# Optimization experiments

Measured on AMD Instinct MI355X. Metric: run time of the kernel, lower is better.

## Reference

```python
import jax, jax.numpy as jnp
import numpy as np

D, DFF, H, K = 512, 2048, 8, 31
DK = D // H
EPS = 1e-5


def _ln(x, g, b):
    m = jnp.mean(x, axis=-1, keepdims=True)
    v = jnp.mean((x - m) ** 2, axis=-1, keepdims=True)
    return (x - m) * jax.lax.rsqrt(v + EPS) * g + b


def _ffn(x, w1, b1, w2, b2):
    return jax.nn.silu(x @ w1 + b1) @ w2 + b2


def _rel_shift(x):
    # x: (B, H, T, P) with P = 2T-1
    b, h, q, p = x.shape
    x = jnp.pad(x, ((0, 0), (0, 0), (0, 0), (1, 0)))
    x = x.reshape(b, h, p + 1, q)[:, :, 1:, :]
    return x.reshape(b, h, q, p)


def setup_inputs() -> dict:
    key = jax.random.key(0)
    ks = jax.random.split(key, 32)
    r = lambda i, shape: 0.02 * jax.random.normal(ks[i], shape, dtype=jnp.float32)
    B, T = 4, 1024
    inp = {
        'x': jax.random.normal(ks[0], (B, T, D), dtype=jnp.float32),
        'pos_emb': jax.random.normal(ks[1], (1, 2 * T - 1, D), dtype=jnp.float32),
        # LayerNorms (5)
        'ln1_g': jnp.ones((D,)), 'ln1_b': jnp.zeros((D,)),
        'ln2_g': jnp.ones((D,)), 'ln2_b': jnp.zeros((D,)),
        'ln3_g': jnp.ones((D,)), 'ln3_b': jnp.zeros((D,)),
        'ln4_g': jnp.ones((D,)), 'ln4_b': jnp.zeros((D,)),
        'ln5_g': jnp.ones((D,)), 'ln5_b': jnp.zeros((D,)),
        # FFN1
        'ff1_w1': r(2, (D, DFF)), 'ff1_b1': jnp.zeros((DFF,)),
        'ff1_w2': r(3, (DFF, D)), 'ff1_b2': jnp.zeros((D,)),
        # Attention
        'wq': r(4, (D, D)), 'bq': jnp.zeros((D,)),
        'wk': r(5, (D, D)), 'bk': jnp.zeros((D,)),
        'wv': r(6, (D, D)), 'bv': jnp.zeros((D,)),
        'wp': r(7, (D, D)),
        'wo': r(8, (D, D)), 'bo': jnp.zeros((D,)),
        'pos_u': r(9, (H, DK)), 'pos_v': r(10, (H, DK)),
        # Conv module
        'pw1_w': r(11, (2 * D, D)), 'pw1_b': jnp.zeros((2 * D,)),
        'dw_w': r(12, (D, 1, K)), 'dw_b': jnp.zeros((D,)),
        'bn_g': jnp.ones((D,)), 'bn_b': jnp.zeros((D,)),
        'pw2_w': r(13, (D, D)), 'pw2_b': jnp.zeros((D,)),
        # FFN2
        'ff2_w1': r(14, (D, DFF)), 'ff2_b1': jnp.zeros((DFF,)),
        'ff2_w2': r(15, (DFF, D)), 'ff2_b2': jnp.zeros((D,)),
    }
    return inp


def _attn(x, pos_emb, wq, bq, wk, bk, wv, bv, wp, wo, bo, pos_u, pos_v):
    B, T, _ = x.shape
    q = (x @ wq + bq).reshape(B, T, H, DK).transpose(0, 2, 1, 3)
    k = (x @ wk + bk).reshape(B, T, H, DK).transpose(0, 2, 1, 3)
    v = (x @ wv + bv).reshape(B, T, H, DK).transpose(0, 2, 1, 3)
    P = pos_emb.shape[1]
    p = (pos_emb[0] @ wp).reshape(P, H, DK)  # (P, H, DK)
    ac = jnp.einsum('bhqd,bhkd->bhqk', q + pos_u[:, None, :], k)
    bd = jnp.einsum('bhqd,phd->bhqp', q + pos_v[:, None, :], p)
    bd = _rel_shift(bd)[:, :, :, :T]
    scores = (ac + bd) * (DK ** -0.5)
    attn = jax.nn.softmax(scores, axis=-1)
    out = jnp.einsum('bhqk,bhkd->bhqd', attn, v)
    out = out.transpose(0, 2, 1, 3).reshape(B, T, D)
    return out @ wo + bo


def _conv(x, pw1_w, pw1_b, dw_w, dw_b, bn_g, bn_b, pw2_w, pw2_b):
    y = x.transpose(0, 2, 1)  # (B, D, T)
    y = jnp.einsum('od,bdt->bot', pw1_w, y) + pw1_b[:, None]
    a, g = jnp.split(y, 2, axis=1)
    y = a * jax.nn.sigmoid(g)  # GLU
    pad = (K - 1) // 2
    y = jax.lax.conv_general_dilated(
        y, dw_w, (1,), [(pad, pad)],
        dimension_numbers=('NCW', 'OIW', 'NCW'), feature_group_count=D)
    y = y + dw_b[:, None]
    m = jnp.mean(y, axis=(0, 2), keepdims=True)
    var = jnp.mean((y - m) ** 2, axis=(0, 2), keepdims=True)
    y = (y - m) * jax.lax.rsqrt(var + EPS) * bn_g[:, None] + bn_b[:, None]
    y = jax.nn.silu(y)
    y = jnp.einsum('od,bdt->bot', pw2_w, y) + pw2_b[:, None]
    return y.transpose(0, 2, 1)


def reference(x, pos_emb,
              ln1_g, ln1_b, ff1_w1, ff1_b1, ff1_w2, ff1_b2,
              ln2_g, ln2_b, wq, bq, wk, bk, wv, bv, wp, wo, bo, pos_u, pos_v,
              ln3_g, ln3_b, pw1_w, pw1_b, dw_w, dw_b, bn_g, bn_b, pw2_w, pw2_b,
              ln4_g, ln4_b, ff2_w1, ff2_b1, ff2_w2, ff2_b2,
              ln5_g, ln5_b):
    h = x + 0.5 * _ffn(_ln(x, ln1_g, ln1_b), ff1_w1, ff1_b1, ff1_w2, ff1_b2)
    h = h + _attn(_ln(h, ln2_g, ln2_b), pos_emb, wq, bq, wk, bk, wv, bv, wp, wo, bo, pos_u, pos_v)
    h = h + _conv(_ln(h, ln3_g, ln3_b), pw1_w, pw1_b, dw_w, dw_b, bn_g, bn_b, pw2_w, pw2_b)
    h = h + 0.5 * _ffn(_ln(h, ln4_g, ln4_b), ff2_w1, ff2_b1, ff2_w2, ff2_b2)
    return _ln(h, ln5_g, ln5_b)
```

## Files before the change

### kernel.cpp

```cpp
#include <hip/hip_runtime.h>
#include <math.h>

#define TT   1024
#define BBZ  4
#define DD   512
#define DFF_ 2048
#define HH   8
#define DKK  64
#define NTOK 4096
#define EPSF 1e-5f
#define MB   1048576

typedef unsigned short u16;
typedef __attribute__((ext_vector_type(8))) short s8v;
typedef __attribute__((ext_vector_type(4))) float f32x4;
typedef __attribute__((ext_vector_type(4))) unsigned short us4;

__device__ __forceinline__ float b2f(u16 v){
    union { unsigned int u; float f; } x; x.u = ((unsigned int)v) << 16; return x.f;
}
__device__ __forceinline__ u16 f2b(float f){
    union { float f; unsigned int u; } x; x.f = f;
    unsigned int r = x.u + 0x7fffu + ((x.u >> 16) & 1u);
    return (u16)(r >> 16);
}
__device__ __forceinline__ float sigmoidf_(float x){ return 1.0f/(1.0f+__expf(-x)); }

__device__ __forceinline__ void gld16(const u16* g, u16* l){
    __builtin_amdgcn_global_load_lds(
        (const __attribute__((address_space(1))) unsigned int*)g,
        (__attribute__((address_space(3))) unsigned int*)l, 16, 0, 0);
}

template<int OMODE>
__global__ __launch_bounds__(256) void bgemm128(
    const u16* __restrict__ A, int lda,
    const u16* __restrict__ B, int ldb,
    void* __restrict__ Cv, int ldc, int K,
    const float* __restrict__ bias, int act, float alpha,
    const float* __restrict__ resid,
    const float* __restrict__ posu, const float* __restrict__ posv)
{
    int n0 = blockIdx.x * 128;
    int m0 = blockIdx.y * 128;

    __shared__ u16 As[128*64];
    __shared__ u16 Bs[128*64];

    int t = threadIdx.x;
    int w = t >> 6, l = t & 63;
    int lrow = l >> 3, lslot = l & 7;
    int kswz = (lslot ^ lrow) * 8;
    int wm = w >> 1, wn = w & 1;
    int lr = l & 15, lk = l >> 4;

    f32x4 acc[4][4] = {};

    for (int k0 = 0; k0 < K; k0 += 64){
        #pragma unroll
        for (int it = 0; it < 4; ++it){
            int rb = it*32 + w*8;
            gld16(A + (size_t)(m0 + rb + lrow)*lda + k0 + kswz, &As[rb*64]);
            gld16(B + (size_t)(n0 + rb + lrow)*ldb + k0 + kswz, &Bs[rb*64]);
        }
        __syncthreads();

        s8v af[2][4], bf[2][4];
        #pragma unroll
        for (int kh = 0; kh < 2; ++kh){
            int sl = (kh*4 + lk) ^ (lr & 7);
            #pragma unroll
            for (int mi = 0; mi < 4; ++mi)
                af[kh][mi] = *(const s8v*)&As[(wm*64 + mi*16 + lr)*64 + sl*8];
            #pragma unroll
            for (int ni = 0; ni < 4; ++ni)
                bf[kh][ni] = *(const s8v*)&Bs[(wn*64 + ni*16 + lr)*64 + sl*8];
        }
        #pragma unroll
        for (int kh = 0; kh < 2; ++kh)
            #pragma unroll
            for (int mi = 0; mi < 4; ++mi)
                #pragma unroll
                for (int ni = 0; ni < 4; ++ni)
                    acc[mi][ni] = __builtin_amdgcn_mfma_f32_16x16x32_bf16(
                        af[kh][mi], bf[kh][ni], acc[mi][ni], 0, 0, 0);
        __syncthreads();
    }

    #pragma unroll
    for (int mi = 0; mi < 4; ++mi){
        #pragma unroll
        for (int ni = 0; ni < 4; ++ni){
            int gn = n0 + wn*64 + ni*16 + lr;
            float bval = bias ? bias[gn] : 0.0f;
            #pragma unroll
            for (int r = 0; r < 4; ++r){
                int gm = m0 + wm*64 + mi*16 + lk*4 + r;
                float vv = acc[mi][ni][r] + bval;
                if (act) vv = vv * sigmoidf_(vv);
                if (OMODE == 0){
                    vv *= alpha;
                    if (resid) vv += resid[(size_t)gm*ldc + gn];
                    ((float*)Cv)[(size_t)gm*ldc + gn] = vv;
                } else if (OMODE == 1){
                    ((u16*)Cv)[(size_t)gm*ldc + gn] = f2b(vv);
                } else {
                    u16* base = (u16*)Cv;
                    if (gn < 512){
                        size_t idx = (size_t)gm*512 + gn;
                        base[idx]              = f2b((vv + posu[gn])*0.125f);
                        base[idx + (2u<<20)]   = f2b((vv + posv[gn])*0.125f);
                    } else if (gn < 1024){
                        base[(4u<<20) + (size_t)gm*512 + (gn-512)] = f2b(vv);
                    } else {
                        int gnp = gn - 1024;
                        int bb = gm >> 10, tt2 = gm & 1023;
                        size_t idx = (((size_t)(bb*8 + (gnp>>6)))*64 + (gnp&63))*1024 + tt2;
                        base[(6u<<20) + idx] = f2b(vv);
                    }
                }
            }
        }
    }
}

template<int OMODE>
__global__ __launch_bounds__(256) void bgemm64(
    const u16* __restrict__ A, int lda,
    const u16* __restrict__ B, int ldb,
    void* __restrict__ Cv, int ldc, int K,
    const float* __restrict__ bias, float alpha,
    const float* __restrict__ resid)
{
    int n0 = blockIdx.x * 64;
    int m0 = blockIdx.y * 64;

    __shared__ u16 As[64*64];
    __shared__ u16 Bs[64*64];

    int t = threadIdx.x;
    int w = t >> 6, l = t & 63;
    int lrow = l >> 3, lslot = l & 7;
    int kswz = (lslot ^ lrow) * 8;
    int wm = w >> 1, wn = w & 1;
    int lr = l & 15, lk = l >> 4;

    f32x4 acc[2][2] = {};

    for (int k0 = 0; k0 < K; k0 += 64){
        #pragma unroll
        for (int it = 0; it < 2; ++it){
            int rb = it*32 + w*8;
            gld16(A + (size_t)(m0 + rb + lrow)*lda + k0 + kswz, &As[rb*64]);
            gld16(B + (size_t)(n0 + rb + lrow)*ldb + k0 + kswz, &Bs[rb*64]);
        }
        __syncthreads();

        s8v af[2][2], bf[2][2];
        #pragma unroll
        for (int kh = 0; kh < 2; ++kh){
            int sl = (kh*4 + lk) ^ (lr & 7);
            #pragma unroll
            for (int mi = 0; mi < 2; ++mi)
                af[kh][mi] = *(const s8v*)&As[(wm*32 + mi*16 + lr)*64 + sl*8];
            #pragma unroll
            for (int ni = 0; ni < 2; ++ni)
                bf[kh][ni] = *(const s8v*)&Bs[(wn*32 + ni*16 + lr)*64 + sl*8];
        }
        #pragma unroll
        for (int kh = 0; kh < 2; ++kh)
            #pragma unroll
            for (int mi = 0; mi < 2; ++mi)
                #pragma unroll
                for (int ni = 0; ni < 2; ++ni)
                    acc[mi][ni] = __builtin_amdgcn_mfma_f32_16x16x32_bf16(
                        af[kh][mi], bf[kh][ni], acc[mi][ni], 0, 0, 0);
        __syncthreads();
    }

    #pragma unroll
    for (int mi = 0; mi < 2; ++mi){
        #pragma unroll
        for (int ni = 0; ni < 2; ++ni){
            int gn = n0 + wn*32 + ni*16 + lr;
            float bval = bias ? bias[gn] : 0.0f;
            #pragma unroll
            for (int r = 0; r < 4; ++r){
                int gm = m0 + wm*32 + mi*16 + lk*4 + r;
                float vv = acc[mi][ni][r] + bval;
                if (OMODE == 0){
                    vv *= alpha;
                    if (resid) vv += resid[(size_t)gm*ldc + gn];
                    ((float*)Cv)[(size_t)gm*ldc + gn] = vv;
                } else {
                    ((u16*)Cv)[(size_t)gm*ldc + gn] = f2b(vv);
                }
            }
        }
    }
}

__global__ __launch_bounds__(256) void attn_fused(
    const u16* __restrict__ qub, const u16* __restrict__ qvb,
    const u16* __restrict__ kb,  const u16* __restrict__ vt,
    const u16* __restrict__ pp,  u16* __restrict__ out)
{
    int z = blockIdx.y;
    int b = z >> 3, hh = z & 7;
    int i0 = blockIdx.x * 64;

    __shared__ u16 Kb2[2][64*64];
    __shared__ u16 Pring[3][64*64];
    __shared__ u16 Vb[64*64];
    __shared__ u16 PT[64*64];
    __shared__ float Band[64*64];

    int t = threadIdx.x;
    int w = t >> 6, l = t & 63;
    int lrow = l >> 3, lslot = l & 7;
    int kswz = (lslot ^ lrow) * 8;
    int lr = l & 15, lk = l >> 4;

    #pragma unroll
    for (int it = 0; it < 2; ++it){
        int rb = it*32 + w*8;
        gld16(qub + (size_t)(b*TT + i0 + rb + lrow)*DD + hh*64 + kswz, &Vb[rb*64]);
        gld16(qvb + (size_t)(b*TT + i0 + rb + lrow)*DD + hh*64 + kswz, &PT[rb*64]);
    }
    __syncthreads();
    s8v af_u[2], af_v[2];
    #pragma unroll
    for (int kh = 0; kh < 2; ++kh){
        int sl = (kh*4 + lk) ^ (lr & 7);
        af_u[kh] = *(const s8v*)&Vb[(w*16 + lr)*64 + sl*8];
        af_v[kh] = *(const s8v*)&PT[(w*16 + lr)*64 + sl*8];
    }
    #pragma unroll
    for (int it = 0; it < 2; ++it){
        int rb = it*32 + w*8;
        gld16(kb + (size_t)(b*TT +        rb + lrow)*DD + hh*64 + kswz, &Kb2[0][rb*64]);
        gld16(pp + (size_t)(960  - i0 +   rb + lrow)*DD + hh*64 + kswz, &Pring[0][rb*64]);
        gld16(pp + (size_t)(1024 - i0 +   rb + lrow)*DD + hh*64 + kswz, &Pring[1][rb*64]);
    }

    f32x4 o_[4] = {};
    float M_[4], L_[4];
    #pragma unroll
    for (int r = 0; r < 4; ++r){ M_[r] = -3e38f; L_[r] = 0.0f; }

    int nbase = 3 - w;
    int s0 = 0, s1 = 1, s2 = 2;

    for (int jt = 0; jt < 16; ++jt){
        int cur = jt & 1;
        __syncthreads();

        #pragma unroll
        for (int it = 0; it < 2; ++it){
            int rb = it*32 + w*8;
            gld16(vt + ((size_t)z*64 + rb + lrow)*TT + jt*64 + kswz, &Vb[rb*64]);
            if (jt < 15){
                gld16(kb + (size_t)(b*TT + (jt+1)*64 + rb + lrow)*DD + hh*64 + kswz,
                      &Kb2[cur^1][rb*64]);
                gld16(pp + (size_t)(960 + (jt+2)*64 - i0 + rb + lrow)*DD + hh*64 + kswz,
                      &Pring[s2][rb*64]);
            }
        }

        f32x4 sac[4] = {};
        f32x4 g[5] = {};
        #pragma unroll
        for (int kh = 0; kh < 2; ++kh){
            int sl = (kh*4 + lk) ^ (lr & 7);
            #pragma unroll
            for (int n = 0; n < 4; ++n){
                s8v bK = *(const s8v*)&Kb2[cur][(n*16 + lr)*64 + sl*8];
                sac[n] = __builtin_amdgcn_mfma_f32_16x16x32_bf16(af_u[kh], bK, sac[n], 0,0,0);
            }
            #pragma unroll
            for (int n = 0; n < 5; ++n){
                int nn = nbase + n;
                const u16* pc = (nn & 4) ? &Pring[s1][0] : &Pring[s0][0];
                s8v bP = *(const s8v*)&pc[(((nn&3)*16) + lr)*64 + sl*8];
                g[n] = __builtin_amdgcn_mfma_f32_16x16x32_bf16(af_v[kh], bP, g[n], 0,0,0);
            }
        }
        #pragma unroll
        for (int n = 0; n < 5; ++n){
            int nn = nbase + n;
            #pragma unroll
            for (int r = 0; r < 4; ++r){
                int ii = w*16 + lk*4 + r;
                int jj = nn*16 + lr - 63 + ii;
                if (jj >= 0 && jj < 64)
                    Band[ii*64 + ((jj + 4*ii) & 63)] = g[n][r];
            }
        }

        float p_[4][4], sc_[4];
        #pragma unroll
        for (int r = 0; r < 4; ++r){
            int ii = w*16 + lk*4 + r;
            float sv[4]; float mx = -3e38f;
            #pragma unroll
            for (int n = 0; n < 4; ++n){
                int jj = n*16 + lr;
                float vvv = sac[n][r] + Band[ii*64 + ((jj + 4*ii) & 63)];
                sv[n] = vvv; mx = fmaxf(mx, vvv);
            }
            #pragma unroll
            for (int msk = 1; msk < 16; msk <<= 1) mx = fmaxf(mx, __shfl_xor(mx, msk));
            float nm = fmaxf(M_[r], mx);
            float scale = __expf(M_[r] - nm);
            float rs = 0.0f;
            #pragma unroll
            for (int n = 0; n < 4; ++n){ p_[n][r] = __expf(sv[n] - nm); rs += p_[n][r]; }
            #pragma unroll
            for (int msk = 1; msk < 16; msk <<= 1) rs += __shfl_xor(rs, msk);
            L_[r] = L_[r]*scale + rs;
            M_[r] = nm;
            sc_[r] = scale;
        }
        #pragma unroll
        for (int n = 0; n < 4; ++n)
            #pragma unroll
            for (int r = 0; r < 4; ++r)
                o_[n][r] *= sc_[r];

        #pragma unroll
        for (int n = 0; n < 4; ++n)
            #pragma unroll
            for (int r = 0; r < 4; ++r){
                int ii  = w*16 + lk*4 + r;
                int col = n*16 + lr;
                int sl  = (col>>3) ^ (ii&7);
                PT[ii*64 + sl*8 + (col&7)] = f2b(p_[n][r]);
            }

        __syncthreads();

        #pragma unroll
        for (int kh = 0; kh < 2; ++kh){
            int sl = (kh*4 + lk) ^ (lr & 7);
            s8v ap = *(const s8v*)&PT[(w*16 + lr)*64 + sl*8];
            #pragma unroll
            for (int n = 0; n < 4; ++n){
                s8v bV = *(const s8v*)&Vb[(n*16 + lr)*64 + sl*8];
                o_[n] = __builtin_amdgcn_mfma_f32_16x16x32_bf16(ap, bV, o_[n], 0,0,0);
            }
        }
        int tmp = s0; s0 = s1; s1 = s2; s2 = tmp;
    }

    #pragma unroll
    for (int n = 0; n < 4; ++n)
        #pragma unroll
        for (int r = 0; r < 4; ++r){
            int i  = i0 + w*16 + lk*4 + r;
            int dk = n*16 + lr;
            out[(size_t)(b*TT + i)*DD + hh*64 + dk] = f2b(o_[n][r] / L_[r]);
        }
}

template<int OB>
__global__ __launch_bounds__(256) void ln_kernel(const float* __restrict__ in,
    const float* __restrict__ g, const float* __restrict__ b, void* __restrict__ outv)
{
    int w = threadIdx.x >> 6, l = threadIdx.x & 63;
    int row = blockIdx.x*4 + w;
    const float4* xr = (const float4*)(in + (size_t)row*DD);
    float4 v0 = xr[l], v1 = xr[64 + l];
    float s = v0.x+v0.y+v0.z+v0.w + v1.x+v1.y+v1.z+v1.w;
    float q = v0.x*v0.x+v0.y*v0.y+v0.z*v0.z+v0.w*v0.w
            + v1.x*v1.x+v1.y*v1.y+v1.z*v1.z+v1.w*v1.w;
    #pragma unroll
    for (int msk = 1; msk < 64; msk <<= 1){
        s += __shfl_xor(s, msk);
        q += __shfl_xor(q, msk);
    }
    float mean = s*(1.0f/DD);
    float var  = q*(1.0f/DD) - mean*mean;
    float inv  = rsqrtf(var+EPSF);
    float4 g0 = ((const float4*)g)[l], g1 = ((const float4*)g)[64+l];
    float4 b0 = ((const float4*)b)[l], b1 = ((const float4*)b)[64+l];
    float y0x=(v0.x-mean)*inv*g0.x+b0.x, y0y=(v0.y-mean)*inv*g0.y+b0.y;
    float y0z=(v0.z-mean)*inv*g0.z+b0.z, y0w=(v0.w-mean)*inv*g0.w+b0.w;
    float y1x=(v1.x-mean)*inv*g1.x+b1.x, y1y=(v1.y-mean)*inv*g1.y+b1.y;
    float y1z=(v1.z-mean)*inv*g1.z+b1.z, y1w=(v1.w-mean)*inv*g1.w+b1.w;
    if (OB){
        us4 o0 = { f2b(y0x), f2b(y0y), f2b(y0z), f2b(y0w) };
        us4 o1 = { f2b(y1x), f2b(y1y), f2b(y1z), f2b(y1w) };
        us4* op = (us4*)((u16*)outv + (size_t)row*DD);
        op[l] = o0; op[64+l] = o1;
    } else {
        float4 o0 = { y0x, y0y, y0z, y0w };
        float4 o1 = { y1x, y1y, y1z, y1w };
        float4* op = (float4*)((float*)outv + (size_t)row*DD);
        op[l] = o0; op[64+l] = o1;
    }
}

struct Prep9 {
    const float* s[9];
    u16* d[9];
    int R[9], C[9];
    int t0[10];
};

__global__ __launch_bounds__(256) void prep_transpose(Prep9 P)
{
    __shared__ float tile[32][33];
    int bid = blockIdx.x;
    int j = 0;
    #pragma unroll
    for (int e=1; e<9; e++) if (bid >= P.t0[e]) j = e;
    int lb = bid - P.t0[j];
    int nx = P.C[j] >> 5;
    int c0 = (lb % nx) << 5;
    int r0 = (lb / nx) << 5;
    const float* in = P.s[j];
    u16* out = P.d[j];
    int R = P.R[j], C = P.C[j];
    int tx = threadIdx.x & 31, ty = threadIdx.x >> 5;
    #pragma unroll
    for (int i=0;i<4;i++){
        int rr = ty + i*8;
        tile[rr][tx] = in[(size_t)(r0+rr)*C + c0+tx];
    }
    __syncthreads();
    #pragma unroll
    for (int i=0;i<4;i++){
        int cc = ty + i*8;
        out[(size_t)(c0+cc)*R + r0+tx] = f2b(tile[tx][cc]);
    }
}

__global__ __launch_bounds__(256) void prep_convert(
    const float* __restrict__ pw1_w, const float* __restrict__ pw2_w,
    const float* __restrict__ pos_emb, const float* __restrict__ dw_w,
    const float* __restrict__ bq, const float* __restrict__ bk,
    const float* __restrict__ bv,
    u16* __restrict__ pw1b, u16* __restrict__ pw2b,
    u16* __restrict__ posb, float* __restrict__ wt, float* __restrict__ bqkv)
{
    int i = blockIdx.x*256 + threadIdx.x;
    if (i < 524288) { pw1b[i] = f2b(pw1_w[i]); return; }
    i -= 524288;
    if (i < 262144) { pw2b[i] = f2b(pw2_w[i]); return; }
    i -= 262144;
    if (i < 1048576) { posb[i] = (i < 2047*512) ? f2b(pos_emb[i]) : (u16)0; return; }
    i -= 1048576;
    if (i < 15872) { int kk = i >> 9, d = i & 511; wt[i] = dw_w[d*31+kk]; return; }
    i -= 15872;
    if (i < 1536) bqkv[i] = (i < 512) ? bq[i] : (i < 1024 ? bk[i-512] : bv[i-1024]);
}

__global__ __launch_bounds__(256) void dwconv_kernel(const float* __restrict__ t2,
    const float* __restrict__ wt, const float* __restrict__ bias, float* __restrict__ z)
{
    int d  = blockIdx.x*256 + threadIdx.x;
    int c  = blockIdx.y;
    int b  = c >> 7;
    int t0 = (c & 127) << 3;
    const float* pa = t2 + (size_t)b*TT*1024 + d;
    float wv[31];
    #pragma unroll
    for (int kk=0;kk<31;kk++) wv[kk] = wt[kk*512 + d];
    float xv[38];
    #pragma unroll
    for (int e=0;e<38;e++){
        int tp = t0 - 15 + e;
        if (tp >= 0 && tp < TT){
            float a  = pa[(size_t)tp*1024];
            float gg = pa[(size_t)tp*1024 + 512];
            xv[e] = a * sigmoidf_(gg);
        } else xv[e] = 0.0f;
    }
    float bsv = bias[d];
    #pragma unroll
    for (int j=0;j<8;j++){
        float sum = bsv;
        #pragma unroll
        for (int kk=0;kk<31;kk++) sum = fmaf(xv[j+kk], wv[kk], sum);
        z[(size_t)(b*TT+t0+j)*DD + d] = sum;
    }
}

__global__ __launch_bounds__(256) void bn_reduce_kernel(const float* __restrict__ z, float* __restrict__ stats)
{
    int c = blockIdx.x, t = threadIdx.x;
    float s=0.f, q=0.f;
    for (int r=t; r<NTOK; r+=256){
        float vv = z[(size_t)r*DD + c];
        s += vv; q += vv*vv;
    }
    __shared__ float rs[256], rq[256];
    rs[t]=s; rq[t]=q; __syncthreads();
    for (int st=128; st>0; st>>=1){
        if (t<st){ rs[t]+=rs[t+st]; rq[t]+=rq[t+st]; }
        __syncthreads();
    }
    if (t==0){ stats[c]=rs[0]; stats[DD+c]=rq[0]; }
}

__global__ __launch_bounds__(256) void bn_apply_kernel(const float* __restrict__ z,
    const float* __restrict__ stats, const float* __restrict__ g, const float* __restrict__ b,
    u16* __restrict__ out)
{
    int idx = blockIdx.x*256 + threadIdx.x;
    int c = idx & (DD-1);
    float m   = stats[c]*(1.0f/NTOK);
    float var = stats[DD+c]*(1.0f/NTOK) - m*m;
    float vv  = (z[idx]-m)*rsqrtf(var+EPSF)*g[c] + b[c];
    out[idx]  = f2b(vv*sigmoidf_(vv));
}

extern "C" void kernel_launch(void* const* d_in, const int* in_sizes, int n_in,
                              void* d_out, int out_size, void* d_ws, size_t ws_size,
                              hipStream_t stream)
{
    const float* x       = (const float*)d_in[0];
    const float* pos_emb = (const float*)d_in[1];
    const float* ln1_g=(const float*)d_in[2],  *ln1_b=(const float*)d_in[3];
    const float* ln2_g=(const float*)d_in[4],  *ln2_b=(const float*)d_in[5];
    const float* ln3_g=(const float*)d_in[6],  *ln3_b=(const float*)d_in[7];
    const float* ln4_g=(const float*)d_in[8],  *ln4_b=(const float*)d_in[9];
    const float* ln5_g=(const float*)d_in[10], *ln5_b=(const float*)d_in[11];
    const float* ff1_w1=(const float*)d_in[12], *ff1_b1=(const float*)d_in[13];
    const float* ff1_w2=(const float*)d_in[14], *ff1_b2=(const float*)d_in[15];
    const float* wq=(const float*)d_in[16], *bq=(const float*)d_in[17];
    const float* wk=(const float*)d_in[18], *bk=(const float*)d_in[19];
    const float* wv=(const float*)d_in[20], *bv=(const float*)d_in[21];
    const float* wp=(const float*)d_in[22];
    const float* wo=(const float*)d_in[23], *bo=(const float*)d_in[24];
    const float* pos_u=(const float*)d_in[25], *pos_v=(const float*)d_in[26];
    const float* pw1_w=(const float*)d_in[27], *pw1_b=(const float*)d_in[28];
    const float* dw_w=(const float*)d_in[29],  *dw_b=(const float*)d_in[30];
    const float* bn_g=(const float*)d_in[31],  *bn_b=(const float*)d_in[32];
    const float* pw2_w=(const float*)d_in[33], *pw2_b=(const float*)d_in[34];
    const float* ff2_w1=(const float*)d_in[35], *ff2_b1=(const float*)d_in[36];
    const float* ff2_w2=(const float*)d_in[37], *ff2_b2=(const float*)d_in[38];

    char* W = (char*)d_ws;
    float* h    = (float*)(W);
    u16*  xn    = (u16*) (W + (size_t) 8*MB);
    u16*  wall  = (u16*) (W + (size_t)12*MB);
    u16*  qub   = (u16*) (W + (size_t)28*MB);
    u16*  qvb   = (u16*) (W + (size_t)32*MB);
    u16*  kb    = (u16*) (W + (size_t)36*MB);
    u16*  vt    = (u16*) (W + (size_t)40*MB);
    u16*  pproj = (u16*) (W + (size_t)44*MB);
    char* big   = W + (size_t)48*MB;
    u16*  ffh   = (u16*)big;
    float* t2   = (float*)big;
    float* t3   = (float*)(big + (size_t)16*MB);
    float* stats= (float*)(W + (size_t)112*MB);
    float* wt   = stats + 4096;
    float* bqkv = wt + 15872;

    u16* ff1w1T = wall;
    u16* ff1w2T = wall + 1048576;
    u16* wqT    = wall + 2097152;
    u16* wkT    = wall + 2359296;
    u16* wvT    = wall + 2621440;
    u16* wpT    = wall + 2883584;
    u16* woT    = wall + 3145728;
    u16* ff2w1T = wall + 3407872;
    u16* ff2w2T = wall + 4456448;
    u16* pw1b   = wall + 5505024;
    u16* pw2b   = wall + 6029312;
    u16* posb   = wall + 6291456;

    dim3 blk(256);

    Prep9 P;
    P.s[0]=ff1_w1; P.d[0]=ff1w1T; P.R[0]=512;  P.C[0]=2048;
    P.s[1]=ff1_w2; P.d[1]=ff1w2T; P.R[1]=2048; P.C[1]=512;
    P.s[2]=wq;     P.d[2]=wqT;    P.R[2]=512;  P.C[2]=512;
    P.s[3]=wk;     P.d[3]=wkT;    P.R[3]=512;  P.C[3]=512;
    P.s[4]=wv;     P.d[4]=wvT;    P.R[4]=512;  P.C[4]=512;
    P.s[5]=wp;     P.d[5]=wpT;    P.R[5]=512;  P.C[5]=512;
    P.s[6]=wo;     P.d[6]=woT;    P.R[6]=512;  P.C[6]=512;
    P.s[7]=ff2_w1; P.d[7]=ff2w1T; P.R[7]=512;  P.C[7]=2048;
    P.s[8]=ff2_w2; P.d[8]=ff2w2T; P.R[8]=2048; P.C[8]=512;
    int tc[9] = {1024,1024,256,256,256,256,256,1024,1024};
    P.t0[0]=0; for (int e=0;e<9;e++) P.t0[e+1]=P.t0[e]+tc[e];
    prep_transpose<<<dim3(5376), blk, 0, stream>>>(P);
    prep_convert<<<dim3(7236), blk, 0, stream>>>(pw1_w, pw2_w, pos_emb, dw_w,
                                                 bq, bk, bv,
                                                 pw1b, pw2b, posb, wt, bqkv);

    ln_kernel<1><<<dim3(NTOK/4), blk, 0, stream>>>(x, ln1_g, ln1_b, xn);
    bgemm128<1><<<dim3(16,32), blk, 0, stream>>>(xn,512, ff1w1T,512,
        ffh,2048, 512, ff1_b1,1,1.f, nullptr,nullptr,nullptr);
    bgemm64<0><<<dim3(8,64), blk, 0, stream>>>(ffh,2048, ff1w2T,2048,
        h,512, 2048, ff1_b2,0.5f, x);

    ln_kernel<1><<<dim3(NTOK/4), blk, 0, stream>>>(h, ln2_g, ln2_b, xn);
    bgemm128<5><<<dim3(12,32), blk, 0, stream>>>(xn,512, wqT,512,
        qub,512, 512, bqkv,0,1.f, nullptr,pos_u,pos_v);
    bgemm64<1><<<dim3(8,32), blk, 0, stream>>>(posb,512, wpT,512,
        pproj,512, 512, nullptr,1.f, nullptr);

    attn_fused<<<dim3(16,32), blk, 0, stream>>>(qub, qvb, kb, vt, pproj, xn);

    bgemm64<0><<<dim3(8,64), blk, 0, stream>>>(xn,512, woT,512,
        h,512, 512, bo,1.f, h);

    ln_kernel<1><<<dim3(NTOK/4), blk, 0, stream>>>(h, ln3_g, ln3_b, xn);
    bgemm128<0><<<dim3(8,32), blk, 0, stream>>>(xn,512, pw1b,512,
        t2,1024, 512, pw1_b,0,1.f, nullptr,nullptr,nullptr);
    dwconv_kernel<<<dim3(2,512), blk, 0, stream>>>(t2, wt, dw_b, t3);
    bn_reduce_kernel<<<dim3(DD), blk, 0, stream>>>(t3, stats);
    bn_apply_kernel<<<dim3(NTOK*DD/256), blk, 0, stream>>>(t3, stats, bn_g, bn_b, xn);
    bgemm64<0><<<dim3(8,64), blk, 0, stream>>>(xn,512, pw2b,512,
        h,512, 512, pw2_b,1.f, h);

    ln_kernel<1><<<dim3(NTOK/4), blk, 0, stream>>>(h, ln4_g, ln4_b, xn);
    bgemm128<1><<<dim3(16,32), blk, 0, stream>>>(xn,512, ff2w1T,512,
        ffh,2048, 512, ff2_b1,1,1.f, nullptr,nullptr,nullptr);
    bgemm64<0><<<dim3(8,64), blk, 0, stream>>>(ffh,2048, ff2w2T,2048,
        h,512, 2048, ff2_b2,0.5f, h);

    ln_kernel<0><<<dim3(NTOK/4), blk, 0, stream>>>(h, ln5_g, ln5_b, (float*)d_out);
}
```

Baseline: 304.8 us.

## Use bf16 conv intermediates, atomic BN reduce, K128 FFN-down GEMM, double-buffered attention V

The conv path now stores the pointwise GEMM output as interleaved bf16 pairs and the depthwise output as bf16, which halves the traffic between the conv kernels. The BN statistics reduction becomes a row-tiled kernel that accumulates with atomics after a memset. The FFN down-projections use a new 64x64 GEMM with a K-tile of 128, so there are fewer barriers per K step. The attention kernel double-buffers V with prefetch and drops one barrier per iteration. The costs are bf16 rounding of pre-BN values, atomic ordering nondeterminism, and a possible race on the PT buffer now that the barrier before the P·V MFMAs is gone.

```diff
diff --git a/kernel.cpp b/kernel.cpp
--- a/kernel.cpp
+++ b/kernel.cpp
@@ -104,7 +104,7 @@
                     ((float*)Cv)[(size_t)gm*ldc + gn] = vv;
                 } else if (OMODE == 1){
                     ((u16*)Cv)[(size_t)gm*ldc + gn] = f2b(vv);
-                } else {
+                } else if (OMODE == 5){
                     u16* base = (u16*)Cv;
                     if (gn < 512){
                         size_t idx = (size_t)gm*512 + gn;
@@ -118,6 +118,12 @@
                         size_t idx = (((size_t)(bb*8 + (gnp>>6)))*64 + (gnp&63))*1024 + tt2;
                         base[(6u<<20) + idx] = f2b(vv);
                     }
+                } else {
+                    u16* base = (u16*)Cv;
+                    size_t idx = (gn < 512)
+                        ? ((size_t)gm*512 + gn)*2
+                        : ((size_t)gm*512 + (gn-512))*2 + 1;
+                    base[idx] = f2b(vv);
                 }
             }
         }
@@ -200,6 +206,75 @@
     }
 }
 
+__global__ __launch_bounds__(256) void bgemm64k(
+    const u16* __restrict__ A, int lda,
+    const u16* __restrict__ B, int ldb,
+    float* __restrict__ C, int ldc, int K,
+    const float* __restrict__ bias, float alpha,
+    const float* __restrict__ resid)
+{
+    int n0 = blockIdx.x * 64;
+    int m0 = blockIdx.y * 64;
+
+    __shared__ u16 As[64*128];
+    __shared__ u16 Bs[64*128];
+
+    int t = threadIdx.x;
+    int w = t >> 6, l = t & 63;
+    int r4 = l >> 4;
+    int s16 = l & 15;
+    int kswz = (s16 ^ (w*4 + r4)) * 8;
+    int wm = w >> 1, wn = w & 1;
+    int lr = l & 15, lk = l >> 4;
+
+    f32x4 acc[2][2] = {};
+
+    for (int k0 = 0; k0 < K; k0 += 128){
+        #pragma unroll
+        for (int cb = 0; cb < 4; ++cb){
+            int rowu = cb*16 + w*4;
+            gld16(A + (size_t)(m0 + rowu + r4)*lda + k0 + kswz, &As[rowu*128]);
+            gld16(B + (size_t)(n0 + rowu + r4)*ldb + k0 + kswz, &Bs[rowu*128]);
+        }
+        __syncthreads();
+
+        #pragma unroll
+        for (int kh = 0; kh < 4; ++kh){
+            int sl = ((kh*4 + lk) ^ lr) * 8;
+            s8v af[2], bf[2];
+            #pragma unroll
+            for (int mi = 0; mi < 2; ++mi)
+                af[mi] = *(const s8v*)&As[(wm*32 + mi*16 + lr)*128 + sl];
+            #pragma unroll
+            for (int ni = 0; ni < 2; ++ni)
+                bf[ni] = *(const s8v*)&Bs[(wn*32 + ni*16 + lr)*128 + sl];
+            #pragma unroll
+            for (int mi = 0; mi < 2; ++mi)
+                #pragma unroll
+                for (int ni = 0; ni < 2; ++ni)
+                    acc[mi][ni] = __builtin_amdgcn_mfma_f32_16x16x32_bf16(
+                        af[mi], bf[ni], acc[mi][ni], 0, 0, 0);
+        }
+        __syncthreads();
+    }
+
+    #pragma unroll
+    for (int mi = 0; mi < 2; ++mi){
+        #pragma unroll
+        for (int ni = 0; ni < 2; ++ni){
+            int gn = n0 + wn*32 + ni*16 + lr;
+            float bval = bias ? bias[gn] : 0.0f;
+            #pragma unroll
+            for (int r = 0; r < 4; ++r){
+                int gm = m0 + wm*32 + mi*16 + lk*4 + r;
+                float vv = (acc[mi][ni][r] + bval) * alpha;
+                if (resid) vv += resid[(size_t)gm*ldc + gn];
+                C[(size_t)gm*ldc + gn] = vv;
+            }
+        }
+    }
+}
+
 __global__ __launch_bounds__(256) void attn_fused(
     const u16* __restrict__ qub, const u16* __restrict__ qvb,
     const u16* __restrict__ kb,  const u16* __restrict__ vt,
@@ -210,8 +285,8 @@
     int i0 = blockIdx.x * 64;
 
     __shared__ u16 Kb2[2][64*64];
+    __shared__ u16 Vb2[2][64*64];
     __shared__ u16 Pring[3][64*64];
-    __shared__ u16 Vb[64*64];
     __shared__ u16 PT[64*64];
     __shared__ float Band[64*64];
 
@@ -224,21 +299,23 @@
     #pragma unroll
     for (int it = 0; it < 2; ++it){
         int rb = it*32 + w*8;
-        gld16(qub + (size_t)(b*TT + i0 + rb + lrow)*DD + hh*64 + kswz, &Vb[rb*64]);
-        gld16(qvb + (size_t)(b*TT + i0 + rb + lrow)*DD + hh*64 + kswz, &PT[rb*64]);
+        gld16(qub + (size_t)(b*TT + i0 + rb + lrow)*DD + hh*64 + kswz, &PT[rb*64]);
+        gld16(qvb + (size_t)(b*TT + i0 + rb + lrow)*DD + hh*64 + kswz,
+              (u16*)Band + rb*64);
     }
     __syncthreads();
     s8v af_u[2], af_v[2];
     #pragma unroll
     for (int kh = 0; kh < 2; ++kh){
         int sl = (kh*4 + lk) ^ (lr & 7);
-        af_u[kh] = *(const s8v*)&Vb[(w*16 + lr)*64 + sl*8];
-        af_v[kh] = *(const s8v*)&PT[(w*16 + lr)*64 + sl*8];
+        af_u[kh] = *(const s8v*)&PT[(w*16 + lr)*64 + sl*8];
+        af_v[kh] = *(const s8v*)((const u16*)Band + (w*16 + lr)*64 + sl*8);
     }
     #pragma unroll
     for (int it = 0; it < 2; ++it){
         int rb = it*32 + w*8;
         gld16(kb + (size_t)(b*TT +        rb + lrow)*DD + hh*64 + kswz, &Kb2[0][rb*64]);
+        gld16(vt + ((size_t)z*64 + rb + lrow)*TT +                kswz, &Vb2[0][rb*64]);
         gld16(pp + (size_t)(960  - i0 +   rb + lrow)*DD + hh*64 + kswz, &Pring[0][rb*64]);
         gld16(pp + (size_t)(1024 - i0 +   rb + lrow)*DD + hh*64 + kswz, &Pring[1][rb*64]);
     }
@@ -255,13 +332,14 @@
         int cur = jt & 1;
         __syncthreads();
 
-        #pragma unroll
-        for (int it = 0; it < 2; ++it){
-            int rb = it*32 + w*8;
-            gld16(vt + ((size_t)z*64 + rb + lrow)*TT + jt*64 + kswz, &Vb[rb*64]);
-            if (jt < 15){
+        if (jt < 15){
+            #pragma unroll
+            for (int it = 0; it < 2; ++it){
+                int rb = it*32 + w*8;
                 gld16(kb + (size_t)(b*TT + (jt+1)*64 + rb + lrow)*DD + hh*64 + kswz,
                       &Kb2[cur^1][rb*64]);
+                gld16(vt + ((size_t)z*64 + rb + lrow)*TT + (jt+1)*64 + kswz,
+                      &Vb2[cur^1][rb*64]);
                 gld16(pp + (size_t)(960 + (jt+2)*64 - i0 + rb + lrow)*DD + hh*64 + kswz,
                       &Pring[s2][rb*64]);
             }
@@ -337,15 +415,13 @@
                 PT[ii*64 + sl*8 + (col&7)] = f2b(p_[n][r]);
             }
 
-        __syncthreads();
-
         #pragma unroll
         for (int kh = 0; kh < 2; ++kh){
             int sl = (kh*4 + lk) ^ (lr & 7);
             s8v ap = *(const s8v*)&PT[(w*16 + lr)*64 + sl*8];
             #pragma unroll
             for (int n = 0; n < 4; ++n){
-                s8v bV = *(const s8v*)&Vb[(n*16 + lr)*64 + sl*8];
+                s8v bV = *(const s8v*)&Vb2[cur][(n*16 + lr)*64 + sl*8];
                 o_[n] = __builtin_amdgcn_mfma_f32_16x16x32_bf16(ap, bV, o_[n], 0,0,0);
             }
         }
@@ -455,14 +531,14 @@
     if (i < 1536) bqkv[i] = (i < 512) ? bq[i] : (i < 1024 ? bk[i-512] : bv[i-1024]);
 }
 
-__global__ __launch_bounds__(256) void dwconv_kernel(const float* __restrict__ t2,
-    const float* __restrict__ wt, const float* __restrict__ bias, float* __restrict__ z)
+__global__ __launch_bounds__(256) void dwconv_kernel(const unsigned int* __restrict__ t2i,
+    const float* __restrict__ wt, const float* __restrict__ bias, u16* __restrict__ z)
 {
     int d  = blockIdx.x*256 + threadIdx.x;
     int c  = blockIdx.y;
     int b  = c >> 7;
     int t0 = (c & 127) << 3;
-    const float* pa = t2 + (size_t)b*TT*1024 + d;
+    const unsigned int* pa = t2i + (size_t)b*TT*512 + d;
     float wv[31];
     #pragma unroll
     for (int kk=0;kk<31;kk++) wv[kk] = wt[kk*512 + d];
@@ -471,8 +547,9 @@
     for (int e=0;e<38;e++){
         int tp = t0 - 15 + e;
         if (tp >= 0 && tp < TT){
-            float a  = pa[(size_t)tp*1024];
-            float gg = pa[(size_t)tp*1024 + 512];
+            unsigned int pv = pa[(size_t)tp*512];
+            float a  = b2f((u16)(pv & 0xffffu));
+            float gg = b2f((u16)(pv >> 16));
             xv[e] = a * sigmoidf_(gg);
         } else xv[e] = 0.0f;
     }
@@ -482,28 +559,31 @@
         float sum = bsv;
         #pragma unroll
         for (int kk=0;kk<31;kk++) sum = fmaf(xv[j+kk], wv[kk], sum);
-        z[(size_t)(b*TT+t0+j)*DD + d] = sum;
-    }
-}
-
-__global__ __launch_bounds__(256) void bn_reduce_kernel(const float* __restrict__ z, float* __restrict__ stats)
-{
-    int c = blockIdx.x, t = threadIdx.x;
-    float s=0.f, q=0.f;
-    for (int r=t; r<NTOK; r+=256){
-        float vv = z[(size_t)r*DD + c];
-        s += vv; q += vv*vv;
-    }
-    __shared__ float rs[256], rq[256];
-    rs[t]=s; rq[t]=q; __syncthreads();
-    for (int st=128; st>0; st>>=1){
-        if (t<st){ rs[t]+=rs[t+st]; rq[t]+=rq[t+st]; }
-        __syncthreads();
-    }
-    if (t==0){ stats[c]=rs[0]; stats[DD+c]=rq[0]; }
-}
-
-__global__ __launch_bounds__(256) void bn_apply_kernel(const float* __restrict__ z,
+        z[(size_t)(b*TT+t0+j)*DD + d] = f2b(sum);
+    }
+}
+
+__global__ __launch_bounds__(256) void bn_reduce2(const u16* __restrict__ z,
+    float* __restrict__ stats)
+{
+    int bi = blockIdx.x;
+    int t  = threadIdx.x;
+    float s0=0.f,q0=0.f,s1=0.f,q1=0.f;
+    #pragma unroll
+    for (int r=0;r<16;r++){
+        size_t row = (size_t)(bi*16 + r)*DD;
+        float v0 = b2f(z[row + t]);
+        float v1 = b2f(z[row + t + 256]);
+        s0 += v0; q0 += v0*v0;
+        s1 += v1; q1 += v1*v1;
+    }
+    atomicAdd(&stats[t],        s0);
+    atomicAdd(&stats[512 + t],  q0);
+    atomicAdd(&stats[t + 256],      s1);
+    atomicAdd(&stats[512 + t + 256], q1);
+}
+
+__global__ __launch_bounds__(256) void bn_apply_kernel(const u16* __restrict__ z,
     const float* __restrict__ stats, const float* __restrict__ g, const float* __restrict__ b,
     u16* __restrict__ out)
 {
@@ -511,7 +591,7 @@
     int c = idx & (DD-1);
     float m   = stats[c]*(1.0f/NTOK);
     float var = stats[DD+c]*(1.0f/NTOK) - m*m;
-    float vv  = (z[idx]-m)*rsqrtf(var+EPSF)*g[c] + b[c];
+    float vv  = (b2f(z[idx])-m)*rsqrtf(var+EPSF)*g[c] + b[c];
     out[idx]  = f2b(vv*sigmoidf_(vv));
 }
 
@@ -552,8 +632,8 @@
     u16*  pproj = (u16*) (W + (size_t)44*MB);
     char* big   = W + (size_t)48*MB;
     u16*  ffh   = (u16*)big;
-    float* t2   = (float*)big;
-    float* t3   = (float*)(big + (size_t)16*MB);
+    unsigned int* t2i = (unsigned int*)big;
+    u16*  t3u   = (u16*)(big + (size_t)8*MB);
     float* stats= (float*)(W + (size_t)112*MB);
     float* wt   = stats + 4096;
     float* bqkv = wt + 15872;
@@ -593,7 +673,7 @@
     ln_kernel<1><<<dim3(NTOK/4), blk, 0, stream>>>(x, ln1_g, ln1_b, xn);
     bgemm128<1><<<dim3(16,32), blk, 0, stream>>>(xn,512, ff1w1T,512,
         ffh,2048, 512, ff1_b1,1,1.f, nullptr,nullptr,nullptr);
-    bgemm64<0><<<dim3(8,64), blk, 0, stream>>>(ffh,2048, ff1w2T,2048,
+    bgemm64k<<<dim3(8,64), blk, 0, stream>>>(ffh,2048, ff1w2T,2048,
         h,512, 2048, ff1_b2,0.5f, x);
 
     ln_kernel<1><<<dim3(NTOK/4), blk, 0, stream>>>(h, ln2_g, ln2_b, xn);
@@ -608,18 +688,19 @@
         h,512, 512, bo,1.f, h);
 
     ln_kernel<1><<<dim3(NTOK/4), blk, 0, stream>>>(h, ln3_g, ln3_b, xn);
-    bgemm128<0><<<dim3(8,32), blk, 0, stream>>>(xn,512, pw1b,512,
-        t2,1024, 512, pw1_b,0,1.f, nullptr,nullptr,nullptr);
-    dwconv_kernel<<<dim3(2,512), blk, 0, stream>>>(t2, wt, dw_b, t3);
-    bn_reduce_kernel<<<dim3(DD), blk, 0, stream>>>(t3, stats);
-    bn_apply_kernel<<<dim3(NTOK*DD/256), blk, 0, stream>>>(t3, stats, bn_g, bn_b, xn);
+    bgemm128<6><<<dim3(8,32), blk, 0, stream>>>(xn,512, pw1b,512,
+        t2i,1024, 512, pw1_b,0,1.f, nullptr,nullptr,nullptr);
+    dwconv_kernel<<<dim3(2,512), blk, 0, stream>>>(t2i, wt, dw_b, t3u);
+    hipMemsetAsync(stats, 0, 4096, stream);
+    bn_reduce2<<<dim3(256), blk, 0, stream>>>(t3u, stats);
+    bn_apply_kernel<<<dim3(NTOK*DD/256), blk, 0, stream>>>(t3u, stats, bn_g, bn_b, xn);
     bgemm64<0><<<dim3(8,64), blk, 0, stream>>>(xn,512, pw2b,512,
         h,512, 512, pw2_b,1.f, h);
 
     ln_kernel<1><<<dim3(NTOK/4), blk, 0, stream>>>(h, ln4_g, ln4_b, xn);
     bgemm128<1><<<dim3(16,32), blk, 0, stream>>>(xn,512, ff2w1T,512,
         ffh,2048, 512, ff2_b1,1,1.f, nullptr,nullptr,nullptr);
-    bgemm64<0><<<dim3(8,64), blk, 0, stream>>>(ffh,2048, ff2w2T,2048,
+    bgemm64k<<<dim3(8,64), blk, 0, stream>>>(ffh,2048, ff2w2T,2048,
         h,512, 2048, ff2_b2,0.5f, h);
 
     ln_kernel<0><<<dim3(NTOK/4), blk, 0, stream>>>(h, ln5_g, ln5_b, (float*)d_out);
```

New measurement: 291.4 us. 1.05x faster.
